# Performance work log

Hardware: AMD Instinct MI355X
Metric: run time of the kernel (lower is better)

## Reference

```python
import jax, jax.numpy as jnp
import numpy as np

DIM = 256
NUM_HEADS = 8
HEAD_DIM = DIM // NUM_HEADS
SCALE = 1.0 / DIM ** 0.5  # NOTE: source scales by 1/sqrt(dim), not 1/sqrt(head_dim)


def setup_inputs() -> dict:
    key = jax.random.key(0)
    k_x, k_wqkv, k_wout = jax.random.split(key, 3)
    x = jax.random.normal(k_x, (4, 2048, DIM), dtype=jnp.float32)
    # xavier_uniform for Linear(dim, 3*dim): limit = sqrt(6/(fan_in+fan_out))
    lim_qkv = float(np.sqrt(6.0 / (DIM + 3 * DIM)))
    w_qkv = jax.random.uniform(k_wqkv, (3 * DIM, DIM), minval=-lim_qkv, maxval=lim_qkv, dtype=jnp.float32)
    b_qkv = jnp.zeros((3 * DIM,), dtype=jnp.float32)
    lim_out = float(np.sqrt(6.0 / (DIM + DIM)))
    w_out = jax.random.uniform(k_wout, (DIM, DIM), minval=-lim_out, maxval=lim_out, dtype=jnp.float32)
    b_out = jnp.zeros((DIM,), dtype=jnp.float32)
    return {"x": x, "w_qkv": w_qkv, "b_qkv": b_qkv, "w_out": w_out, "b_out": b_out}


def reference(x, w_qkv, b_qkv, w_out, b_out):
    B, N, C = x.shape
    H, D = NUM_HEADS, C // NUM_HEADS
    qkv = x @ w_qkv.T + b_qkv                       # [B, N, 3C]
    qkv = qkv.reshape(B, N, 3, H, D)
    q = qkv[:, :, 0].transpose(0, 2, 1, 3)          # [B, H, N, D]
    k = qkv[:, :, 1].transpose(0, 2, 1, 3)
    v = qkv[:, :, 2].transpose(0, 2, 1, 3)
    attn = jnp.einsum("bhnd,bhmd->bhnm", q, k) * SCALE  # [B, H, N, N]
    attn = jax.nn.softmax(attn, axis=-1)
    z = jnp.einsum("bhnm,bhmd->bhnd", attn, v)      # [B, H, N, D]
    z = z.transpose(0, 2, 1, 3).reshape(B, N, C)
    return z @ w_out.T + b_out
```

## Files before the change

kernel.cpp:

```cpp
#include <hip/hip_runtime.h>


#define SEQ 2048
#define BATCH 4
#define NHEADS 8
#define HDIM 32
#define DIMC 256
#define SCALE_LOG2E 0.09016844005556021f

typedef __attribute__((ext_vector_type(8))) short short8;
typedef __attribute__((ext_vector_type(4))) float f32x4;

union BF8 { unsigned u[4]; short8 s8; };

__device__ __forceinline__ unsigned pk2bf(float a, float b) {
    union { float f; unsigned u; } ua, ub;
    ua.f = a; ub.f = b;
    return __builtin_amdgcn_perm(ub.u + 0x8000u, ua.u + 0x8000u, 0x07060302u);
}
__device__ __forceinline__ short f2bf(float a) {
    union { float f; unsigned u; } x; x.f = a;
    return (short)((x.u + 0x8000u) >> 16);
}

#define NX (BATCH * SEQ * DIMC)
#define NQW (3 * DIMC * DIMC)
#define NOW (DIMC * DIMC)

__global__ __launch_bounds__(256) void cvt_bf16(const float* __restrict__ x,
                                                const float* __restrict__ wq,
                                                const float* __restrict__ wo,
                                                short* __restrict__ xb,
                                                short* __restrict__ wqb,
                                                short* __restrict__ wob) {
    int i = (blockIdx.x * 256 + threadIdx.x) * 4;
    const float* src;
    short* dst;
    int off;
    if (i < NX) { src = x; dst = xb; off = i; }
    else if (i < NX + NQW) { src = wq; dst = wqb; off = i - NX; }
    else { src = wo; dst = wob; off = i - NX - NQW; }
    float4 v = *(const float4*)&src[off];
    uint2 p;
    p.x = pk2bf(v.x, v.y);
    p.y = pk2bf(v.z, v.w);
    *(uint2*)&dst[off] = p;
}

__global__ __launch_bounds__(256) void qkv_mfma(const short* __restrict__ Xb,
                                                const short* __restrict__ Wb,
                                                const float* __restrict__ bias,
                                                short* __restrict__ Q,
                                                short* __restrict__ Kd,
                                                short* __restrict__ V) {
    __shared__ __align__(16) union SM {
        struct { short A[128][72]; short B[128][72]; } ab;
        short C[128][136];
    } sm;
    const int m0 = blockIdx.y * 128, bx = blockIdx.x;
    const int tid = threadIdx.x;
    const int w = tid >> 6, lane = tid & 63;
    const int m = lane & 15, g = lane >> 4;
    const int wr = w >> 1, wc = w & 1;
    const int srow = tid >> 1, scol = (tid & 1) * 32;

    f32x4 acc[4][4] = {};

    for (int kt = 0; kt < DIMC; kt += 64) {
        short8 a8[4], b8[4];
#pragma unroll
        for (int i = 0; i < 4; i++) {
            a8[i] = *(const short8*)&Xb[(size_t)(m0 + srow) * DIMC + kt + scol + i * 8];
            b8[i] = *(const short8*)&Wb[(size_t)(bx * 128 + srow) * DIMC + kt + scol + i * 8];
        }
        __syncthreads();
#pragma unroll
        for (int i = 0; i < 4; i++) {
            *(short8*)&sm.ab.A[srow][scol + i * 8] = a8[i];
            *(short8*)&sm.ab.B[srow][scol + i * 8] = b8[i];
        }
        __syncthreads();
#pragma unroll
        for (int kk = 0; kk < 2; kk++) {
            short8 af[4], bf[4];
#pragma unroll
            for (int mt = 0; mt < 4; mt++) af[mt] = *(const short8*)&sm.ab.A[wr * 64 + mt * 16 + m][kk * 32 + g * 8];
#pragma unroll
            for (int nt = 0; nt < 4; nt++) bf[nt] = *(const short8*)&sm.ab.B[wc * 64 + nt * 16 + m][kk * 32 + g * 8];
#pragma unroll
            for (int mt = 0; mt < 4; mt++)
#pragma unroll
                for (int nt = 0; nt < 4; nt++)
                    acc[mt][nt] = __builtin_amdgcn_mfma_f32_16x16x32_bf16(af[mt], bf[nt], acc[mt][nt], 0, 0, 0);
        }
    }

    const int which = bx >> 1;
    const int h0 = (bx & 1) * 4;
    const int bidx = blockIdx.y >> 4;
    const int ntok0 = (blockIdx.y & 15) * 128;
    float bv[4];
#pragma unroll
    for (int nt = 0; nt < 4; nt++) bv[nt] = bias[bx * 128 + wc * 64 + nt * 16 + m];

    __syncthreads();
    if (which != 2) {
        const float qs = (which == 0) ? SCALE_LOG2E : 1.0f;
#pragma unroll
        for (int mt = 0; mt < 4; mt++)
#pragma unroll
            for (int nt = 0; nt < 4; nt++)
#pragma unroll
                for (int r = 0; r < 4; r++)
                    sm.C[wr * 64 + mt * 16 + g * 4 + r][wc * 64 + nt * 16 + m] =
                        f2bf((acc[mt][nt][r] + bv[nt]) * qs);
        __syncthreads();
        short* dst = (which == 0) ? Q : Kd;
        const int tok = tid >> 1, d0 = (tid & 1) * 16;
#pragma unroll
        for (int hh = 0; hh < 4; hh++) {
            size_t o = ((size_t)((bidx * NHEADS + h0 + hh) * SEQ) + ntok0 + tok) * HDIM + d0;
            *(short8*)&dst[o] = *(const short8*)&sm.C[tok][hh * 32 + d0];
            *(short8*)&dst[o + 8] = *(const short8*)&sm.C[tok][hh * 32 + d0 + 8];
        }
    } else {
#pragma unroll
        for (int mt = 0; mt < 4; mt++)
#pragma unroll
            for (int nt = 0; nt < 4; nt++) {
                uint2 p;
                p.x = pk2bf(acc[mt][nt][0] + bv[nt], acc[mt][nt][1] + bv[nt]);
                p.y = pk2bf(acc[mt][nt][2] + bv[nt], acc[mt][nt][3] + bv[nt]);
                *(uint2*)&sm.C[wc * 64 + nt * 16 + m][wr * 64 + mt * 16 + g * 4] = p;
            }
        __syncthreads();
        const int col = tid >> 1, t0 = (tid & 1) * 64;
        const int hh = col >> 5, d = col & 31;
        size_t o = ((size_t)((bidx * NHEADS + h0 + hh) * HDIM) + d) * SEQ + ntok0 + t0;
#pragma unroll
        for (int c2 = 0; c2 < 8; c2++)
            *(short8*)&V[o + c2 * 8] = *(const short8*)&sm.C[col][t0 + c2 * 8];
    }
}

__global__ __launch_bounds__(256) void attn_tile(const short* __restrict__ Q,
                                                 const short* __restrict__ K,
                                                 const short* __restrict__ V,
                                                 short* __restrict__ Zb) {
    __shared__ __align__(16) union SM {
        struct { short Ks[2][128][40]; short Vs[2][32][136]; } kv;
        struct { float O[4][64][36]; float L[4][64]; } ep;
    } sm;

    const int bh = blockIdx.y;
    const int b = bh >> 3, h = bh & 7;
    const int q0 = blockIdx.x * 64;
    const short* qb = Q + (size_t)bh * SEQ * HDIM;
    const short* kb = K + (size_t)bh * SEQ * HDIM;
    const short* vb = V + (size_t)bh * HDIM * SEQ;
    const int tid = threadIdx.x;
    const int w = tid >> 6, lane = tid & 63;
    const int m = lane & 15, g = lane >> 4;

    short8 qfr[4];
#pragma unroll
    for (int qt = 0; qt < 4; qt++)
        qfr[qt] = *(const short8*)(qb + (size_t)(q0 + qt * 16 + m) * HDIM + g * 8);

    const int krow = tid >> 1, kcol = (tid & 1) * 16;
    const int rl = krow & 31;
    const int lrow = (krow & ~31) | (((rl >> 2) & 1) << 4) | ((rl >> 3) << 2) | (rl & 3);
    const int vrow = tid >> 3, vcol = (tid & 7) * 16;

    f32x4 o[4][2] = {};
    f32x4 ol[4] = {};
    const short8 ones = {0x3F80, 0x3F80, 0x3F80, 0x3F80, 0x3F80, 0x3F80, 0x3F80, 0x3F80};

    short8 k0a = *(const short8*)(kb + (size_t)krow * HDIM + kcol);
    short8 k0b = *(const short8*)(kb + (size_t)krow * HDIM + kcol + 8);
    short8 v0a = *(const short8*)(vb + (size_t)vrow * SEQ + vcol);
    short8 v0b = *(const short8*)(vb + (size_t)vrow * SEQ + vcol + 8);
    *(short8*)&sm.kv.Ks[0][lrow][kcol] = k0a;
    *(short8*)&sm.kv.Ks[0][lrow][kcol + 8] = k0b;
    *(short8*)&sm.kv.Vs[0][vrow][vcol] = v0a;
    *(short8*)&sm.kv.Vs[0][vrow][vcol + 8] = v0b;
    __syncthreads();

    for (int it = 0; it < SEQ / 128; ++it) {
        const int buf = it & 1;
        if (it < SEQ / 128 - 1) {
            const int kn = (it + 1) * 128;
            k0a = *(const short8*)(kb + (size_t)(kn + krow) * HDIM + kcol);
            k0b = *(const short8*)(kb + (size_t)(kn + krow) * HDIM + kcol + 8);
            v0a = *(const short8*)(vb + (size_t)vrow * SEQ + kn + vcol);
            v0b = *(const short8*)(vb + (size_t)vrow * SEQ + kn + vcol + 8);
        }

        short8 kf0 = *(const short8*)&sm.kv.Ks[buf][w * 32 + m][g * 8];
        short8 kf1 = *(const short8*)&sm.kv.Ks[buf][w * 32 + 16 + m][g * 8];
        short8 vf0 = *(const short8*)&sm.kv.Vs[buf][m][w * 32 + g * 8];
        short8 vf1 = *(const short8*)&sm.kv.Vs[buf][16 + m][w * 32 + g * 8];

#pragma unroll
        for (int qt = 0; qt < 4; qt++) {
            f32x4 z4 = {0.f, 0.f, 0.f, 0.f};
            f32x4 st0 = __builtin_amdgcn_mfma_f32_16x16x32_bf16(kf0, qfr[qt], z4, 0, 0, 0);
            f32x4 st1 = __builtin_amdgcn_mfma_f32_16x16x32_bf16(kf1, qfr[qt], z4, 0, 0, 0);
            BF8 a;
            a.u[0] = pk2bf(__builtin_amdgcn_exp2f(st0[0]), __builtin_amdgcn_exp2f(st0[1]));
            a.u[1] = pk2bf(__builtin_amdgcn_exp2f(st0[2]), __builtin_amdgcn_exp2f(st0[3]));
            a.u[2] = pk2bf(__builtin_amdgcn_exp2f(st1[0]), __builtin_amdgcn_exp2f(st1[1]));
            a.u[3] = pk2bf(__builtin_amdgcn_exp2f(st1[2]), __builtin_amdgcn_exp2f(st1[3]));
            o[qt][0] = __builtin_amdgcn_mfma_f32_16x16x32_bf16(a.s8, vf0, o[qt][0], 0, 0, 0);
            o[qt][1] = __builtin_amdgcn_mfma_f32_16x16x32_bf16(a.s8, vf1, o[qt][1], 0, 0, 0);
            ol[qt] = __builtin_amdgcn_mfma_f32_16x16x32_bf16(a.s8, ones, ol[qt], 0, 0, 0);
        }

        if (it < SEQ / 128 - 1) {
            const int nb = buf ^ 1;
            *(short8*)&sm.kv.Ks[nb][lrow][kcol] = k0a;
            *(short8*)&sm.kv.Ks[nb][lrow][kcol + 8] = k0b;
            *(short8*)&sm.kv.Vs[nb][vrow][vcol] = v0a;
            *(short8*)&sm.kv.Vs[nb][vrow][vcol + 8] = v0b;
        }
        __syncthreads();
    }

#pragma unroll
    for (int qt = 0; qt < 4; qt++) {
#pragma unroll
        for (int dh = 0; dh < 2; dh++)
#pragma unroll
            for (int r = 0; r < 4; r++)
                sm.ep.O[w][qt * 16 + g * 4 + r][dh * 16 + m] = o[qt][dh][r];
        if (m == 0)
#pragma unroll
            for (int r = 0; r < 4; r++)
                sm.ep.L[w][qt * 16 + g * 4 + r] = ol[qt][r];
    }
    __syncthreads();

    const int ql = tid >> 2, d0 = (tid & 3) * 8;
    float lt = sm.ep.L[0][ql] + sm.ep.L[1][ql] + sm.ep.L[2][ql] + sm.ep.L[3][ql];
    float inv = __builtin_amdgcn_rcpf(lt);
    float sv[8];
#pragma unroll
    for (int j = 0; j < 8; j++)
        sv[j] = sm.ep.O[0][ql][d0 + j] + sm.ep.O[1][ql][d0 + j] +
                sm.ep.O[2][ql][d0 + j] + sm.ep.O[3][ql][d0 + j];
    BF8 pz;
#pragma unroll
    for (int j = 0; j < 4; j++)
        pz.u[j] = pk2bf(sv[2 * j] * inv, sv[2 * j + 1] * inv);
    *(short8*)&Zb[(size_t)(b * SEQ + q0 + ql) * DIMC + h * HDIM + d0] = pz.s8;
}

__global__ __launch_bounds__(256) void out_mfma(const short* __restrict__ A,
                                                const short* __restrict__ Wb,
                                                const float* __restrict__ bias,
                                                float* __restrict__ C) {
    __shared__ __align__(16) short As[128][72];
    __shared__ __align__(16) short Bs[64][72];
    const int m0 = blockIdx.y * 128, n0 = blockIdx.x * 64;
    const int tid = threadIdx.x;
    const int w = tid >> 6, lane = tid & 63;
    const int m = lane & 15, g = lane >> 4;
    const int wr = w >> 1, wc = w & 1;
    const int arow = tid >> 1, acol = (tid & 1) * 32;
    const int brow = tid >> 2, bcol = (tid & 3) * 16;

    f32x4 acc[4][2] = {};

    for (int kt = 0; kt < DIMC; kt += 64) {
        short8 a8[4], b8[2];
#pragma unroll
        for (int i = 0; i < 4; i++)
            a8[i] = *(const short8*)&A[(size_t)(m0 + arow) * DIMC + kt + acol + i * 8];
#pragma unroll
        for (int i = 0; i < 2; i++)
            b8[i] = *(const short8*)&Wb[(size_t)(n0 + brow) * DIMC + kt + bcol + i * 8];
        __syncthreads();
#pragma unroll
        for (int i = 0; i < 4; i++) *(short8*)&As[arow][acol + i * 8] = a8[i];
#pragma unroll
        for (int i = 0; i < 2; i++) *(short8*)&Bs[brow][bcol + i * 8] = b8[i];
        __syncthreads();
#pragma unroll
        for (int kk = 0; kk < 2; kk++) {
            short8 af[4], bf2[2];
#pragma unroll
            for (int mt = 0; mt < 4; mt++) af[mt] = *(const short8*)&As[wr * 64 + mt * 16 + m][kk * 32 + g * 8];
#pragma unroll
            for (int nt = 0; nt < 2; nt++) bf2[nt] = *(const short8*)&Bs[wc * 32 + nt * 16 + m][kk * 32 + g * 8];
#pragma unroll
            for (int mt = 0; mt < 4; mt++)
#pragma unroll
                for (int nt = 0; nt < 2; nt++)
                    acc[mt][nt] = __builtin_amdgcn_mfma_f32_16x16x32_bf16(af[mt], bf2[nt], acc[mt][nt], 0, 0, 0);
        }
    }

    float bv[2];
    bv[0] = bias[n0 + wc * 32 + m];
    bv[1] = bias[n0 + wc * 32 + 16 + m];
#pragma unroll
    for (int mt = 0; mt < 4; mt++)
#pragma unroll
        for (int nt = 0; nt < 2; nt++)
#pragma unroll
            for (int r = 0; r < 4; r++)
                C[(size_t)(m0 + wr * 64 + mt * 16 + g * 4 + r) * DIMC + n0 + wc * 32 + nt * 16 + m] =
                    acc[mt][nt][r] + bv[nt];
}

extern "C" void kernel_launch(void* const* d_in, const int* in_sizes, int n_in,
                              void* d_out, int out_size, void* d_ws, size_t ws_size,
                              hipStream_t stream) {
    const float* x     = (const float*)d_in[0];
    const float* w_qkv = (const float*)d_in[1];
    const float* b_qkv = (const float*)d_in[2];
    const float* w_out = (const float*)d_in[3];
    const float* b_out = (const float*)d_in[4];
    float* out = (float*)d_out;

    const size_t HSZ = (size_t)BATCH * NHEADS * SEQ * HDIM;
    short* xb  = (short*)d_ws;
    short* wqb = xb + NX;
    short* wob = wqb + NQW;
    short* qw  = wob + NOW;
    short* kw  = qw + HSZ;
    short* vw  = kw + HSZ;
    short* zb  = vw + HSZ;

    cvt_bf16<<<(NX + NQW + NOW) / 1024, 256, 0, stream>>>(x, w_qkv, w_out, xb, wqb, wob);
    qkv_mfma<<<dim3(6, 64), 256, 0, stream>>>(xb, wqb, b_qkv, qw, kw, vw);
    attn_tile<<<dim3(32, 32), 256, 0, stream>>>(qw, kw, vw, zb);
    out_mfma<<<dim3(4, 64), 256, 0, stream>>>(zb, wob, b_out, out);
}
```

Before: 122.7 us.

## Fuse fp32-to-bf16 conversion into QKV and output GEMM kernels

Removes the separate conversion kernel and its bf16 copies of x and the weights, so the GEMMs read fp32 directly and convert to bf16 while staging tiles into LDS. The QKV GEMM tile shrinks from 128x128 to 128x64 (768 blocks instead of 384), and the output GEMM goes from 128x64 to 64x64 tiles (512 blocks) to raise parallelism. This saves one launch and a full read/write pass over x, but the QKV kernel now reads fp32 x twice as many times across column blocks, and the smaller tiles reuse less data.

```diff
diff --git a/kernel.cpp b/kernel.cpp
--- a/kernel.cpp
+++ b/kernel.cpp
@@ -23,85 +23,82 @@
     return (short)((x.u + 0x8000u) >> 16);
 }
 
-#define NX (BATCH * SEQ * DIMC)
-#define NQW (3 * DIMC * DIMC)
-#define NOW (DIMC * DIMC)
-
-__global__ __launch_bounds__(256) void cvt_bf16(const float* __restrict__ x,
-                                                const float* __restrict__ wq,
-                                                const float* __restrict__ wo,
-                                                short* __restrict__ xb,
-                                                short* __restrict__ wqb,
-                                                short* __restrict__ wob) {
-    int i = (blockIdx.x * 256 + threadIdx.x) * 4;
-    const float* src;
-    short* dst;
-    int off;
-    if (i < NX) { src = x; dst = xb; off = i; }
-    else if (i < NX + NQW) { src = wq; dst = wqb; off = i - NX; }
-    else { src = wo; dst = wob; off = i - NX - NQW; }
-    float4 v = *(const float4*)&src[off];
-    uint2 p;
-    p.x = pk2bf(v.x, v.y);
-    p.y = pk2bf(v.z, v.w);
-    *(uint2*)&dst[off] = p;
-}
-
-__global__ __launch_bounds__(256) void qkv_mfma(const short* __restrict__ Xb,
-                                                const short* __restrict__ Wb,
-                                                const float* __restrict__ bias,
-                                                short* __restrict__ Q,
-                                                short* __restrict__ Kd,
-                                                short* __restrict__ V) {
+__global__ __launch_bounds__(256) void qkv_fused(const float* __restrict__ X,
+                                                 const float* __restrict__ W,
+                                                 const float* __restrict__ bias,
+                                                 short* __restrict__ Q,
+                                                 short* __restrict__ Kd,
+                                                 short* __restrict__ V) {
     __shared__ __align__(16) union SM {
-        struct { short A[128][72]; short B[128][72]; } ab;
-        short C[128][136];
+        struct { short A[128][72]; short B[64][72]; } ab;
+        short CQ[128][72];
+        short CV[64][136];
     } sm;
+
     const int m0 = blockIdx.y * 128, bx = blockIdx.x;
+    const int n0 = bx * 64;
     const int tid = threadIdx.x;
     const int w = tid >> 6, lane = tid & 63;
     const int m = lane & 15, g = lane >> 4;
     const int wr = w >> 1, wc = w & 1;
-    const int srow = tid >> 1, scol = (tid & 1) * 32;
-
-    f32x4 acc[4][4] = {};
+
+    const int arow = tid >> 1, acol = (tid & 1) * 32;
+    const int brow = tid >> 2, bcol = (tid & 3) * 16;
+
+    f32x4 acc[4][2] = {};
 
     for (int kt = 0; kt < DIMC; kt += 64) {
-        short8 a8[4], b8[4];
+        const float* xp = &X[(size_t)(m0 + arow) * DIMC + kt + acol];
+        const float* wp = &W[(size_t)(n0 + brow) * DIMC + kt + bcol];
+        float4 xv[8], wv[4];
+#pragma unroll
+        for (int i = 0; i < 8; i++) xv[i] = *(const float4*)(xp + i * 4);
+#pragma unroll
+        for (int i = 0; i < 4; i++) wv[i] = *(const float4*)(wp + i * 4);
+        __syncthreads();
 #pragma unroll
         for (int i = 0; i < 4; i++) {
-            a8[i] = *(const short8*)&Xb[(size_t)(m0 + srow) * DIMC + kt + scol + i * 8];
-            b8[i] = *(const short8*)&Wb[(size_t)(bx * 128 + srow) * DIMC + kt + scol + i * 8];
-        }
-        __syncthreads();
-#pragma unroll
-        for (int i = 0; i < 4; i++) {
-            *(short8*)&sm.ab.A[srow][scol + i * 8] = a8[i];
-            *(short8*)&sm.ab.B[srow][scol + i * 8] = b8[i];
+            BF8 c;
+            c.u[0] = pk2bf(xv[i * 2].x, xv[i * 2].y);
+            c.u[1] = pk2bf(xv[i * 2].z, xv[i * 2].w);
+            c.u[2] = pk2bf(xv[i * 2 + 1].x, xv[i * 2 + 1].y);
+            c.u[3] = pk2bf(xv[i * 2 + 1].z, xv[i * 2 + 1].w);
+            *(short8*)&sm.ab.A[arow][acol + i * 8] = c.s8;
+        }
+#pragma unroll
+        for (int i = 0; i < 2; i++) {
+            BF8 c;
+            c.u[0] = pk2bf(wv[i * 2].x, wv[i * 2].y);
+            c.u[1] = pk2bf(wv[i * 2].z, wv[i * 2].w);
+            c.u[2] = pk2bf(wv[i * 2 + 1].x, wv[i * 2 + 1].y);
+            c.u[3] = pk2bf(wv[i * 2 + 1].z, wv[i * 2 + 1].w);
+            *(short8*)&sm.ab.B[brow][bcol + i * 8] = c.s8;
         }
         __syncthreads();
 #pragma unroll
         for (int kk = 0; kk < 2; kk++) {
-            short8 af[4], bf[4];
-#pragma unroll
-            for (int mt = 0; mt < 4; mt++) af[mt] = *(const short8*)&sm.ab.A[wr * 64 + mt * 16 + m][kk * 32 + g * 8];
-#pragma unroll
-            for (int nt = 0; nt < 4; nt++) bf[nt] = *(const short8*)&sm.ab.B[wc * 64 + nt * 16 + m][kk * 32 + g * 8];
+            short8 af[4], bf[2];
 #pragma unroll
             for (int mt = 0; mt < 4; mt++)
-#pragma unroll
-                for (int nt = 0; nt < 4; nt++)
+                af[mt] = *(const short8*)&sm.ab.A[wr * 64 + mt * 16 + m][kk * 32 + g * 8];
+#pragma unroll
+            for (int nt = 0; nt < 2; nt++)
+                bf[nt] = *(const short8*)&sm.ab.B[wc * 32 + nt * 16 + m][kk * 32 + g * 8];
+#pragma unroll
+            for (int mt = 0; mt < 4; mt++)
+#pragma unroll
+                for (int nt = 0; nt < 2; nt++)
                     acc[mt][nt] = __builtin_amdgcn_mfma_f32_16x16x32_bf16(af[mt], bf[nt], acc[mt][nt], 0, 0, 0);
         }
     }
 
-    const int which = bx >> 1;
-    const int h0 = (bx & 1) * 4;
+    const int which = bx >> 2;
+    const int h0 = (bx & 3) * 2;
     const int bidx = blockIdx.y >> 4;
     const int ntok0 = (blockIdx.y & 15) * 128;
-    float bv[4];
-#pragma unroll
-    for (int nt = 0; nt < 4; nt++) bv[nt] = bias[bx * 128 + wc * 64 + nt * 16 + m];
+    float bv[2];
+#pragma unroll
+    for (int nt = 0; nt < 2; nt++) bv[nt] = bias[n0 + wc * 32 + nt * 16 + m];
 
     __syncthreads();
     if (which != 2) {
@@ -109,37 +106,37 @@
 #pragma unroll
         for (int mt = 0; mt < 4; mt++)
 #pragma unroll
-            for (int nt = 0; nt < 4; nt++)
+            for (int nt = 0; nt < 2; nt++)
 #pragma unroll
                 for (int r = 0; r < 4; r++)
-                    sm.C[wr * 64 + mt * 16 + g * 4 + r][wc * 64 + nt * 16 + m] =
+                    sm.CQ[wr * 64 + mt * 16 + g * 4 + r][wc * 32 + nt * 16 + m] =
                         f2bf((acc[mt][nt][r] + bv[nt]) * qs);
         __syncthreads();
         short* dst = (which == 0) ? Q : Kd;
         const int tok = tid >> 1, d0 = (tid & 1) * 16;
 #pragma unroll
-        for (int hh = 0; hh < 4; hh++) {
+        for (int hh = 0; hh < 2; hh++) {
             size_t o = ((size_t)((bidx * NHEADS + h0 + hh) * SEQ) + ntok0 + tok) * HDIM + d0;
-            *(short8*)&dst[o] = *(const short8*)&sm.C[tok][hh * 32 + d0];
-            *(short8*)&dst[o + 8] = *(const short8*)&sm.C[tok][hh * 32 + d0 + 8];
+            *(short8*)&dst[o] = *(const short8*)&sm.CQ[tok][hh * 32 + d0];
+            *(short8*)&dst[o + 8] = *(const short8*)&sm.CQ[tok][hh * 32 + d0 + 8];
         }
     } else {
 #pragma unroll
         for (int mt = 0; mt < 4; mt++)
 #pragma unroll
-            for (int nt = 0; nt < 4; nt++) {
+            for (int nt = 0; nt < 2; nt++) {
                 uint2 p;
                 p.x = pk2bf(acc[mt][nt][0] + bv[nt], acc[mt][nt][1] + bv[nt]);
                 p.y = pk2bf(acc[mt][nt][2] + bv[nt], acc[mt][nt][3] + bv[nt]);
-                *(uint2*)&sm.C[wc * 64 + nt * 16 + m][wr * 64 + mt * 16 + g * 4] = p;
+                *(uint2*)&sm.CV[wc * 32 + nt * 16 + m][wr * 64 + mt * 16 + g * 4] = p;
             }
         __syncthreads();
-        const int col = tid >> 1, t0 = (tid & 1) * 64;
+        const int col = tid >> 2, t0 = (tid & 3) * 32;
         const int hh = col >> 5, d = col & 31;
         size_t o = ((size_t)((bidx * NHEADS + h0 + hh) * HDIM) + d) * SEQ + ntok0 + t0;
 #pragma unroll
-        for (int c2 = 0; c2 < 8; c2++)
-            *(short8*)&V[o + c2 * 8] = *(const short8*)&sm.C[col][t0 + c2 * 8];
+        for (int c2 = 0; c2 < 4; c2++)
+            *(short8*)&V[o + c2 * 8] = *(const short8*)&sm.CV[col][t0 + c2 * 8];
     }
 }
 
@@ -255,62 +252,59 @@
     *(short8*)&Zb[(size_t)(b * SEQ + q0 + ql) * DIMC + h * HDIM + d0] = pz.s8;
 }
 
-__global__ __launch_bounds__(256) void out_mfma(const short* __restrict__ A,
-                                                const short* __restrict__ Wb,
-                                                const float* __restrict__ bias,
-                                                float* __restrict__ C) {
-    __shared__ __align__(16) short As[128][72];
+__global__ __launch_bounds__(256) void out_fused(const short* __restrict__ A,
+                                                 const float* __restrict__ W,
+                                                 const float* __restrict__ bias,
+                                                 float* __restrict__ C) {
+    __shared__ __align__(16) short As[64][72];
     __shared__ __align__(16) short Bs[64][72];
-    const int m0 = blockIdx.y * 128, n0 = blockIdx.x * 64;
+    const int m0 = blockIdx.y * 64, n0 = blockIdx.x * 64;
     const int tid = threadIdx.x;
     const int w = tid >> 6, lane = tid & 63;
     const int m = lane & 15, g = lane >> 4;
-    const int wr = w >> 1, wc = w & 1;
-    const int arow = tid >> 1, acol = (tid & 1) * 32;
-    const int brow = tid >> 2, bcol = (tid & 3) * 16;
-
-    f32x4 acc[4][2] = {};
+    const int srow = tid >> 2, scol = (tid & 3) * 16;
+
+    f32x4 acc[4] = {};
 
     for (int kt = 0; kt < DIMC; kt += 64) {
-        short8 a8[4], b8[2];
-#pragma unroll
-        for (int i = 0; i < 4; i++)
-            a8[i] = *(const short8*)&A[(size_t)(m0 + arow) * DIMC + kt + acol + i * 8];
-#pragma unroll
-        for (int i = 0; i < 2; i++)
-            b8[i] = *(const short8*)&Wb[(size_t)(n0 + brow) * DIMC + kt + bcol + i * 8];
-        __syncthreads();
-#pragma unroll
-        for (int i = 0; i < 4; i++) *(short8*)&As[arow][acol + i * 8] = a8[i];
-#pragma unroll
-        for (int i = 0; i < 2; i++) *(short8*)&Bs[brow][bcol + i * 8] = b8[i];
+        short8 a0 = *(const short8*)&A[(size_t)(m0 + srow) * DIMC + kt + scol];
+        short8 a1 = *(const short8*)&A[(size_t)(m0 + srow) * DIMC + kt + scol + 8];
+        const float* wp = &W[(size_t)(n0 + srow) * DIMC + kt + scol];
+        float4 wv[4];
+#pragma unroll
+        for (int i = 0; i < 4; i++) wv[i] = *(const float4*)(wp + i * 4);
+        __syncthreads();
+        *(short8*)&As[srow][scol] = a0;
+        *(short8*)&As[srow][scol + 8] = a1;
+#pragma unroll
+        for (int i = 0; i < 2; i++) {
+            BF8 c;
+            c.u[0] = pk2bf(wv[i * 2].x, wv[i * 2].y);
+            c.u[1] = pk2bf(wv[i * 2].z, wv[i * 2].w);
+            c.u[2] = pk2bf(wv[i * 2 + 1].x, wv[i * 2 + 1].y);
+            c.u[3] = pk2bf(wv[i * 2 + 1].z, wv[i * 2 + 1].w);
+            *(short8*)&Bs[srow][scol + i * 8] = c.s8;
+        }
         __syncthreads();
 #pragma unroll
         for (int kk = 0; kk < 2; kk++) {
-            short8 af[4], bf2[2];
-#pragma unroll
-            for (int mt = 0; mt < 4; mt++) af[mt] = *(const short8*)&As[wr * 64 + mt * 16 + m][kk * 32 + g * 8];
-#pragma unroll
-            for (int nt = 0; nt < 2; nt++) bf2[nt] = *(const short8*)&Bs[wc * 32 + nt * 16 + m][kk * 32 + g * 8];
-#pragma unroll
-            for (int mt = 0; mt < 4; mt++)
-#pragma unroll
-                for (int nt = 0; nt < 2; nt++)
-                    acc[mt][nt] = __builtin_amdgcn_mfma_f32_16x16x32_bf16(af[mt], bf2[nt], acc[mt][nt], 0, 0, 0);
-        }
-    }
-
-    float bv[2];
-    bv[0] = bias[n0 + wc * 32 + m];
-    bv[1] = bias[n0 + wc * 32 + 16 + m];
-#pragma unroll
-    for (int mt = 0; mt < 4; mt++)
-#pragma unroll
-        for (int nt = 0; nt < 2; nt++)
-#pragma unroll
-            for (int r = 0; r < 4; r++)
-                C[(size_t)(m0 + wr * 64 + mt * 16 + g * 4 + r) * DIMC + n0 + wc * 32 + nt * 16 + m] =
-                    acc[mt][nt][r] + bv[nt];
+            short8 af = *(const short8*)&As[w * 16 + m][kk * 32 + g * 8];
+#pragma unroll
+            for (int nt = 0; nt < 4; nt++) {
+                short8 bf = *(const short8*)&Bs[nt * 16 + m][kk * 32 + g * 8];
+                acc[nt] = __builtin_amdgcn_mfma_f32_16x16x32_bf16(af, bf, acc[nt], 0, 0, 0);
+            }
+        }
+    }
+
+    float bv[4];
+#pragma unroll
+    for (int nt = 0; nt < 4; nt++) bv[nt] = bias[n0 + nt * 16 + m];
+#pragma unroll
+    for (int nt = 0; nt < 4; nt++)
+#pragma unroll
+        for (int r = 0; r < 4; r++)
+            C[(size_t)(m0 + w * 16 + g * 4 + r) * DIMC + n0 + nt * 16 + m] = acc[nt][r] + bv[nt];
 }
 
 extern "C" void kernel_launch(void* const* d_in, const int* in_sizes, int n_in,
@@ -324,16 +318,12 @@
     float* out = (float*)d_out;
 
     const size_t HSZ = (size_t)BATCH * NHEADS * SEQ * HDIM;
-    short* xb  = (short*)d_ws;
-    short* wqb = xb + NX;
-    short* wob = wqb + NQW;
-    short* qw  = wob + NOW;
-    short* kw  = qw + HSZ;
-    short* vw  = kw + HSZ;
-    short* zb  = vw + HSZ;
-
-    cvt_bf16<<<(NX + NQW + NOW) / 1024, 256, 0, stream>>>(x, w_qkv, w_out, xb, wqb, wob);
-    qkv_mfma<<<dim3(6, 64), 256, 0, stream>>>(xb, wqb, b_qkv, qw, kw, vw);
+    short* qw = (short*)d_ws;
+    short* kw = qw + HSZ;
+    short* vw = kw + HSZ;
+    short* zb = vw + HSZ;
+
+    qkv_fused<<<dim3(12, 64), 256, 0, stream>>>(x, w_qkv, b_qkv, qw, kw, vw);
     attn_tile<<<dim3(32, 32), 256, 0, stream>>>(qw, kw, vw, zb);
-    out_mfma<<<dim3(4, 64), 256, 0, stream>>>(zb, wob, b_out, out);
-}
+    out_fused<<<dim3(4, 128), 256, 0, stream>>>(zb, w_out, b_out, out);
+}
```

After: 131.7 us. 7.4% more time.
